# Performance work log

Hardware: AMD Instinct MI355X
Metric: run time of the kernel (lower is better)

## Reference

```python
import jax, jax.numpy as jnp
import numpy as np

K = 3  # kernel_size


def conv2d_same(x, w, b):
    # x: NHWC, w: HWIO
    y = jax.lax.conv_general_dilated(
        x, w, window_strides=(1, 1), padding='SAME',
        dimension_numbers=('NHWC', 'HWIO', 'NHWC'))
    return y + b


def setup_inputs() -> dict:
    key = jax.random.key(0)
    k0, k1, k2 = jax.random.split(key, 3)
    B, H, Wd, C, F = 8, 128, 128, 64, 128
    x = jax.random.normal(k0, (B, H, Wd, C), jnp.float32)
    # offset conv: small random weights (zeros in original init -> degenerate),
    # scaled down so offsets stay in a realistic few-pixel range
    W_off = jax.random.normal(k1, (K, K, C, 2 * K * K), jnp.float32) * 0.01
    b_off = jnp.zeros((2 * K * K,), jnp.float32)
    fan_in = K * K * K * K * C
    W = jax.random.normal(k2, (K, K, K * K * C, F), jnp.float32) / np.float32(np.sqrt(fan_in))
    b = jnp.zeros((F,), jnp.float32)
    return {"x": x, "W_off": W_off, "b_off": b_off, "W": W, "b": b}


def reference(x, W_off, b_off, W, b):
    B, H, Wd, C = x.shape
    KK = K * K
    # predicted per-pixel, per-tap (dx, dy) offsets
    offsets = conv2d_same(x, W_off, b_off).reshape(B, H, Wd, KK, 2)

    # base pixel grid, stacked as (x, y) like the original
    gy, gx = jnp.meshgrid(jnp.arange(H, dtype=jnp.float32),
                          jnp.arange(Wd, dtype=jnp.float32), indexing='ij')
    grid = jnp.stack([gx, gy], axis=-1)[None, :, :, None, :]  # (1,H,W,1,2)

    # kernel tap grid, 'xy' meshgrid like tf.meshgrid default
    off = (K - 1) / 2.0
    lin = jnp.linspace(-off, off, K).astype(jnp.float32)
    kx, ky = jnp.meshgrid(lin, lin)
    kgrid = jnp.stack([kx, ky], axis=-1).reshape(1, 1, 1, KK, 2)

    loc = grid + kgrid + offsets  # (B,H,W,KK,2)
    lx = jnp.clip(loc[..., 0], 0.0, Wd - 1.0)
    ly = jnp.clip(loc[..., 1], 0.0, H - 1.0)

    x0 = jnp.clip(jnp.floor(lx), 0.0, Wd - 1.0)
    x1 = jnp.clip(jnp.floor(lx) + 1.0, 0.0, Wd - 1.0)
    y0 = jnp.clip(jnp.floor(ly), 0.0, H - 1.0)
    y1 = jnp.clip(jnp.floor(ly) + 1.0, 0.0, H - 1.0)

    # weights computed from the CLIPPED corner coords, as in the original
    wa = (x1 - lx) * (y1 - ly)
    wb = (x1 - lx) * (ly - y0)
    wc = (lx - x0) * (y1 - ly)
    wd = (lx - x0) * (ly - y0)

    x0i, x1i = x0.astype(jnp.int32), x1.astype(jnp.int32)
    y0i, y1i = y0.astype(jnp.int32), y1.astype(jnp.int32)

    xf = x.reshape(B, H * Wd, C)

    def gather(yi, xi):
        idx = (yi * Wd + xi).reshape(B, -1)           # (B, H*W*KK)
        g = jax.vmap(lambda f, i: f[i])(xf, idx)      # (B, P, C)
        return g.reshape(B, H, Wd, KK, C)

    Ia = gather(y0i, x0i)
    Ib = gather(y1i, x0i)
    Ic = gather(y0i, x1i)
    Id = gather(y1i, x1i)

    sampled = (wa[..., None] * Ia + wb[..., None] * Ib
               + wc[..., None] * Ic + wd[..., None] * Id)
    sampled = sampled.reshape(B, H, Wd, KK * C)
    return conv2d_same(sampled, W, b)
```

## Files before the change

### kernel.cpp

```cpp
#include <hip/hip_runtime.h>
#include <hip/hip_bf16.h>

#define B_   8
#define H_   128
#define W_   128
#define C_   64
#define F_   128
#define KDIM 5184
#define BHW_ 131072

#define TH   8
#define TW   16
#define HY   10
#define HX   18
#define NPX  180

#define STILE 0
#define BTILE 11520
#define PARMW 36096
#define PARMO 37536
#define LDSSZ 38976

typedef __bf16 bf16x8 __attribute__((ext_vector_type(8)));
typedef float  f32x4  __attribute__((ext_vector_type(4)));

__device__ __forceinline__ unsigned short f2bf(float f) {
  unsigned int u = __float_as_uint(f);
  unsigned int r = (u + 0x7fffu + ((u >> 16) & 1u)) >> 16;
  return (unsigned short)r;
}

__global__ __launch_bounds__(256) void woff_prep_kernel(
    const float* __restrict__ Woff, unsigned short* __restrict__ WbHi,
    unsigned short* __restrict__ WbLo) {
  int u = blockIdx.x * 256 + threadIdx.x;
  if (u >= 18432) return;
  int j  = u & 7;
  int kq = (u >> 3) & 3;
  int n  = (u >> 5) & 15;
  int nt = (u >> 9) & 1;
  int tc = u >> 10;
  int tap = tc >> 1, kch = tc & 1;
  int o = nt * 16 + n;
  int c = kch * 32 + kq * 8 + j;
  float val = 0.f;
  if (o < 18) val = Woff[(tap * 64 + c) * 18 + o];
  unsigned short h = f2bf(val);
  float hf = __uint_as_float((unsigned)h << 16);
  WbHi[u] = h;
  WbLo[u] = f2bf(val - hf);
}

__global__ __launch_bounds__(256, 3) void offs_mfma_kernel(
    const float* __restrict__ x, const unsigned short* __restrict__ WbHi,
    const unsigned short* __restrict__ WbLo, const float* __restrict__ boff,
    float* __restrict__ offsP) {
  __shared__ __align__(16) short lds[26112];
  const int tid = threadIdx.x, lane = tid & 63, w = tid >> 6;
  const int bid = blockIdx.x;
  const int b  = bid >> 7;
  const int t  = bid & 127;
  const int r4 = t >> 2, cq = t & 3;
  const int gy0 = r4 * 4, gx0 = cq * 32;
  const float* xb = x + (size_t)b * (H_ * W_ * C_);

#pragma unroll
  for (int it = 0; it < 7; ++it) {
    int u = it * 256 + tid;
    if (u < 1632) {
      int p = u >> 3, j = u & 7;
      int rowi = p / 34, coli = p - rowi * 34;
      int gy = gy0 - 1 + rowi, gx = gx0 - 1 + coli;
      union { unsigned short s[8]; uint4 v; } hi, lo;
      if ((unsigned)gy < (unsigned)H_ && (unsigned)gx < (unsigned)W_) {
        const float* src = xb + (((gy << 7) + gx) << 6) + j * 8;
        float4 v0 = ((const float4*)src)[0], v1 = ((const float4*)src)[1];
        float f[8] = {v0.x, v0.y, v0.z, v0.w, v1.x, v1.y, v1.z, v1.w};
#pragma unroll
        for (int e = 0; e < 8; ++e) {
          unsigned short h16 = f2bf(f[e]);
          hi.s[e] = h16;
          lo.s[e] = f2bf(f[e] - __uint_as_float((unsigned)h16 << 16));
        }
      } else {
        hi.v = make_uint4(0, 0, 0, 0);
        lo.v = hi.v;
      }
      int a = p * 64 + ((j ^ (coli & 7)) * 8);
      *(uint4*)&lds[a] = hi.v;
      *(uint4*)&lds[13056 + a] = lo.v;
    }
  }
  __syncthreads();

  const int l15 = lane & 15, kq = lane >> 4;
  const int bbase = (l15 * 4 + kq) * 8;
  f32x4 acc[2][2] = {};

#pragma unroll
  for (int ky = 0; ky < 3; ++ky) {
#pragma unroll
    for (int kx = 0; kx < 3; ++kx) {
      const int tap = ky * 3 + kx;
#pragma unroll
      for (int kch = 0; kch < 2; ++kch) {
        const int tc = tap * 2 + kch;
        bf16x8 bh0 = *(const bf16x8*)&WbHi[tc * 1024 + bbase];
        bf16x8 bh1 = *(const bf16x8*)&WbHi[tc * 1024 + 512 + bbase];
        bf16x8 bl0 = *(const bf16x8*)&WbLo[tc * 1024 + bbase];
        bf16x8 bl1 = *(const bf16x8*)&WbLo[tc * 1024 + 512 + bbase];
#pragma unroll
        for (int mt = 0; mt < 2; ++mt) {
          int coli = mt * 16 + l15 + kx;
          int px = (w + ky) * 34 + coli;
          int a = px * 64 + (((kch * 4 + kq) ^ (coli & 7)) * 8);
          bf16x8 ah = *(const bf16x8*)&lds[a];
          bf16x8 al = *(const bf16x8*)&lds[13056 + a];
          acc[mt][0] = __builtin_amdgcn_mfma_f32_16x16x32_bf16(ah, bh0, acc[mt][0], 0, 0, 0);
          acc[mt][0] = __builtin_amdgcn_mfma_f32_16x16x32_bf16(al, bh0, acc[mt][0], 0, 0, 0);
          acc[mt][0] = __builtin_amdgcn_mfma_f32_16x16x32_bf16(ah, bl0, acc[mt][0], 0, 0, 0);
          acc[mt][1] = __builtin_amdgcn_mfma_f32_16x16x32_bf16(ah, bh1, acc[mt][1], 0, 0, 0);
          acc[mt][1] = __builtin_amdgcn_mfma_f32_16x16x32_bf16(al, bh1, acc[mt][1], 0, 0, 0);
          acc[mt][1] = __builtin_amdgcn_mfma_f32_16x16x32_bf16(ah, bl1, acc[mt][1], 0, 0, 0);
        }
      }
    }
  }

  __syncthreads();
  float* accbuf = (float*)lds;
  float bv0 = boff[l15];
  float bv1 = boff[min(16 + l15, 17)];
#pragma unroll
  for (int mt = 0; mt < 2; ++mt)
#pragma unroll
    for (int r = 0; r < 4; ++r) {
      int px = mt * 16 + kq * 4 + r;
      accbuf[(w * 32 + px) * 19 + l15] = acc[mt][0][r] + bv0;
      if (l15 < 2)
        accbuf[(w * 32 + px) * 19 + 16 + l15] = acc[mt][1][r] + bv1;
    }
  __syncthreads();
  const int lane32 = tid & 31, tpi = tid >> 5;
#pragma unroll
  for (int v = 0; v < 9; ++v) {
    int u = v * 8 + tpi;
    int o = u >> 2, w2 = u & 3;
    float val = accbuf[(w2 * 32 + lane32) * 19 + o];
    offsP[(size_t)o * BHW_ + (size_t)b * 16384 + (gy0 + w2) * 128 + gx0 + lane32] = val;
  }
}

__global__ __launch_bounds__(256) void wt_prep_kernel(
    const float* __restrict__ Wf, unsigned short* __restrict__ Wt) {
  __shared__ float Wl[64][65];
  const int tid = threadIdx.x;
  const int kk0 = (blockIdx.x % 81) * 64;
  const int f0  = (blockIdx.x / 81) * 64;
  for (int i = tid; i < 4096; i += 256) {
    int kk = i >> 6, f = i & 63;
    Wl[kk][f] = Wf[(size_t)(kk0 + kk) * F_ + f0 + f];
  }
  __syncthreads();
  for (int i = tid; i < 4096; i += 256) {
    int f = i >> 6, kk = i & 63;
    Wt[(size_t)(f0 + f) * KDIM + kk0 + kk] = f2bf(Wl[kk][f]);
  }
}

__global__ __launch_bounds__(256, 2) void fused_kernel(
    const float* __restrict__ x, const float* __restrict__ offsP,
    const unsigned short* __restrict__ Wt, const float* __restrict__ bias,
    float* __restrict__ out) {
  __shared__ __align__(16) short lds[LDSSZ];
  const int tid  = threadIdx.x;
  const int lane = tid & 63;
  const int wv   = tid >> 6;
  const int gr   = (blockIdx.x & 7) * 128 + (blockIdx.x >> 3);
  const int b    = gr >> 7;
  const int tile = gr & 127;
  const int ty   = tile >> 3, tx = tile & 7;
  const int gy0  = ty * TH, gx0 = tx * TW;
  const float* xb = x + (size_t)b * (H_ * W_ * C_);

  const int l15  = lane & 15, quad = lane >> 4;
  const int sub  = lane & 7,  rig  = lane >> 3;
  const int wn   = (wv & 1) * 64;

  f32x4 acc[4][4] = {};

  int p0[4];
#pragma unroll
  for (int i = 0; i < 4; ++i) p0[i] = ((wv >> 1) * 4 + i) * HX + l15;
  int bo[2][4];
#pragma unroll
  for (int ks = 0; ks < 2; ++ks)
#pragma unroll
    for (int j = 0; j < 4; ++j)
      bo[ks][j] = BTILE + (wn + 16 * j + l15) * 64 + (((ks * 4 + quad) ^ (l15 & 7)) * 8);

  const int s_py = tid / HX, s_px = tid - s_py * HX;

  for (int t = 0; t < 9; ++t) {
    __syncthreads();
#pragma unroll
    for (int i = 0; i < 12; ++i) {
      int slot = wv * 12 + i;
      int chunk = slot >> 4;
      int f = ((slot & 15) * 8) + rig;
      const short* src = (const short*)Wt + (size_t)f * KDIM +
                         chunk * 576 + t * 64 + ((sub ^ rig) * 8);
      __builtin_amdgcn_global_load_lds(
          (const __attribute__((address_space(1))) void*)src,
          (__attribute__((address_space(3))) void*)&lds[BTILE + slot * 512],
          16, 0, 0);
    }
    if (tid < NPX) {
      int gy = gy0 + s_py - 1, gx = gx0 + s_px - 1;
      float wa = 0.f, wb = 0.f, wc = 0.f, wd = 0.f;
      int oA = 0, oB = 0, oC = 0, oD = 0;
      if ((unsigned)gy < (unsigned)H_ && (unsigned)gx < (unsigned)W_) {
        int pix = (b * H_ + gy) * W_ + gx;
        float offx = offsP[(size_t)(2 * t) * BHW_ + pix];
        float offy = offsP[(size_t)(2 * t + 1) * BHW_ + pix];
        float lx = (float)gx + (float)(t % 3 - 1) + offx;
        float ly = (float)gy + (float)(t / 3 - 1) + offy;
        lx = fminf(fmaxf(lx, 0.f), 127.f);
        ly = fminf(fmaxf(ly, 0.f), 127.f);
        float fx = floorf(lx), fy = floorf(ly);
        float x0c = fminf(fmaxf(fx, 0.f), 127.f);
        float x1c = fminf(fmaxf(fx + 1.f, 0.f), 127.f);
        float y0c = fminf(fmaxf(fy, 0.f), 127.f);
        float y1c = fminf(fmaxf(fy + 1.f, 0.f), 127.f);
        wa = (x1c - lx) * (y1c - ly);
        wb = (x1c - lx) * (ly - y0c);
        wc = (lx - x0c) * (y1c - ly);
        wd = (lx - x0c) * (ly - y0c);
        int ix0 = (int)x0c, ix1 = (int)x1c, iy0 = (int)y0c, iy1 = (int)y1c;
        oA = (iy0 * W_ + ix0) * C_;
        oB = (iy1 * W_ + ix0) * C_;
        oC = (iy0 * W_ + ix1) * C_;
        oD = (iy1 * W_ + ix1) * C_;
      }
      ((float4*)&lds[PARMW])[tid] = make_float4(wa, wb, wc, wd);
      ((int4*)&lds[PARMO])[tid]  = make_int4(oA | (s_px << 20), oB, oC, oD);
    }
    __syncthreads();
#pragma unroll
    for (int it = 0; it < 6; ++it) {
      int u = it * 256 + tid;
      if (u < NPX * 8) {
        int p = u >> 3, j = u & 7;
        float4 wv4 = ((const float4*)&lds[PARMW])[p];
        int4   ov4 = ((const int4*)&lds[PARMO])[p];
        int pxl = ov4.x >> 20;
        const float* pa = xb + (ov4.x & 0xFFFFF) + j * 8;
        const float* pb = xb + ov4.y + j * 8;
        const float* pc = xb + ov4.z + j * 8;
        const float* pd = xb + ov4.w + j * 8;
        float4 A0 = ((const float4*)pa)[0], A1 = ((const float4*)pa)[1];
        float4 B0 = ((const float4*)pb)[0], B1 = ((const float4*)pb)[1];
        float4 C0 = ((const float4*)pc)[0], C1 = ((const float4*)pc)[1];
        float4 D0 = ((const float4*)pd)[0], D1 = ((const float4*)pd)[1];
        union { __bf16 h[8]; uint4 v; } uu;
        uu.h[0] = (__bf16)(wv4.x * A0.x + wv4.y * B0.x + wv4.z * C0.x + wv4.w * D0.x);
        uu.h[1] = (__bf16)(wv4.x * A0.y + wv4.y * B0.y + wv4.z * C0.y + wv4.w * D0.y);
        uu.h[2] = (__bf16)(wv4.x * A0.z + wv4.y * B0.z + wv4.z * C0.z + wv4.w * D0.z);
        uu.h[3] = (__bf16)(wv4.x * A0.w + wv4.y * B0.w + wv4.z * C0.w + wv4.w * D0.w);
        uu.h[4] = (__bf16)(wv4.x * A1.x + wv4.y * B1.x + wv4.z * C1.x + wv4.w * D1.x);
        uu.h[5] = (__bf16)(wv4.x * A1.y + wv4.y * B1.y + wv4.z * C1.y + wv4.w * D1.y);
        uu.h[6] = (__bf16)(wv4.x * A1.z + wv4.y * B1.z + wv4.z * C1.z + wv4.w * D1.z);
        uu.h[7] = (__bf16)(wv4.x * A1.w + wv4.y * B1.w + wv4.z * C1.w + wv4.w * D1.w);
        *(uint4*)&lds[STILE + p * 64 + ((j ^ (pxl & 7)) * 8)] = uu.v;
      }
    }
    __syncthreads();

    for (int g = 0; g < 3; ++g) {
      const int off2 = g * HX;
#pragma unroll
      for (int c3 = 0; c3 < 3; ++c3) {
        int t1 = (l15 + c3) & 7;
        int xr0 = ((quad ^ t1) * 8);
        int xr1 = (((4 + quad) ^ t1) * 8);
#pragma unroll
        for (int ks = 0; ks < 2; ++ks) {
          int xr = ks ? xr1 : xr0;
          bf16x8 af[4], bfr[4];
#pragma unroll
          for (int i = 0; i < 4; ++i)
            af[i] = *(const bf16x8*)&lds[(p0[i] + off2 + c3) * 64 + xr];
#pragma unroll
          for (int j = 0; j < 4; ++j)
            bfr[j] = *(const bf16x8*)&lds[bo[ks][j] + c3 * 8192];
#pragma unroll
          for (int i = 0; i < 4; ++i)
#pragma unroll
            for (int j = 0; j < 4; ++j)
              acc[i][j] = __builtin_amdgcn_mfma_f32_16x16x32_bf16(
                  af[i], bfr[j], acc[i][j], 0, 0, 0);
        }
      }
      if (g < 2) {
        __syncthreads();
#pragma unroll
        for (int i = 0; i < 12; ++i) {
          int slot = wv * 12 + i;
          int chunk = slot >> 4;
          int f = ((slot & 15) * 8) + rig;
          int tap2 = (g + 1) * 3 + chunk;
          const short* src = (const short*)Wt + (size_t)f * KDIM +
                             tap2 * 576 + t * 64 + ((sub ^ rig) * 8);
          __builtin_amdgcn_global_load_lds(
              (const __attribute__((address_space(1))) void*)src,
              (__attribute__((address_space(3))) void*)&lds[BTILE + slot * 512],
              16, 0, 0);
        }
        __syncthreads();
      }
    }
  }

  float bj[4];
#pragma unroll
  for (int j = 0; j < 4; ++j) bj[j] = bias[wn + 16 * j + l15];
#pragma unroll
  for (int i = 0; i < 4; ++i) {
    int gy = gy0 + (wv >> 1) * 4 + i;
#pragma unroll
    for (int r = 0; r < 4; ++r) {
      int gx = gx0 + quad * 4 + r;
      float* rp = out + ((size_t)((b * H_ + gy) * W_ + gx)) * F_;
#pragma unroll
      for (int j = 0; j < 4; ++j)
        rp[wn + 16 * j + l15] = acc[i][j][r] + bj[j];
    }
  }
}

extern "C" void kernel_launch(void* const* d_in, const int* in_sizes, int n_in,
                              void* d_out, int out_size, void* d_ws, size_t ws_size,
                              hipStream_t stream) {
  (void)in_sizes; (void)n_in; (void)out_size; (void)ws_size;
  const float* x    = (const float*)d_in[0];
  const float* Woff = (const float*)d_in[1];
  const float* boff = (const float*)d_in[2];
  const float* Wf   = (const float*)d_in[3];
  const float* bias = (const float*)d_in[4];
  float* out = (float*)d_out;

  char* ws = (char*)d_ws;
  size_t off_bytes = (size_t)18 * BHW_ * 4;
  size_t p1 = (off_bytes + 255) & ~(size_t)255;
  size_t wt_bytes = (size_t)F_ * KDIM * 2;
  float*          offsP = (float*)ws;
  unsigned short* Wt    = (unsigned short*)(ws + p1);
  unsigned short* WbHi  = (unsigned short*)(ws + p1 + wt_bytes);
  unsigned short* WbLo  = WbHi + 18432;

  woff_prep_kernel<<<72, 256, 0, stream>>>(Woff, WbHi, WbLo);
  offs_mfma_kernel<<<1024, 256, 0, stream>>>(x, WbHi, WbLo, boff, offsP);
  wt_prep_kernel<<<162, 256, 0, stream>>>(Wf, Wt);
  fused_kernel<<<1024, 256, 0, stream>>>(x, offsP, Wt, bias, out);
}
```

Before: 297.1 us.

## Merge prep kernels, use native bf16 casts, prefetch weight taps into registers

The two weight-preparation kernels are merged into a single launch that splits work by block index, removing one kernel launch. The offset kernel's hi/lo bf16 split now uses native __bf16 conversions instead of the manual rounding helper. In the fused kernel, the next weight-tap group is loaded from global memory into registers before the MFMA loop and written to LDS after the barrier, replacing the direct global-to-LDS loads so the global latency overlaps compute. The register prefetch uses 12 uint4 registers per thread, which can raise register pressure and hurt occupancy under the 2-wave launch bound.

Result: slower. 547.2 us (+84.2%).

```diff
diff --git a/kernel.cpp b/kernel.cpp
--- a/kernel.cpp
+++ b/kernel.cpp
@@ -30,25 +30,43 @@
   return (unsigned short)r;
 }
 
-__global__ __launch_bounds__(256) void woff_prep_kernel(
+__global__ __launch_bounds__(256) void prep_kernel(
     const float* __restrict__ Woff, unsigned short* __restrict__ WbHi,
-    unsigned short* __restrict__ WbLo) {
-  int u = blockIdx.x * 256 + threadIdx.x;
-  if (u >= 18432) return;
-  int j  = u & 7;
-  int kq = (u >> 3) & 3;
-  int n  = (u >> 5) & 15;
-  int nt = (u >> 9) & 1;
-  int tc = u >> 10;
-  int tap = tc >> 1, kch = tc & 1;
-  int o = nt * 16 + n;
-  int c = kch * 32 + kq * 8 + j;
-  float val = 0.f;
-  if (o < 18) val = Woff[(tap * 64 + c) * 18 + o];
-  unsigned short h = f2bf(val);
-  float hf = __uint_as_float((unsigned)h << 16);
-  WbHi[u] = h;
-  WbLo[u] = f2bf(val - hf);
+    unsigned short* __restrict__ WbLo, const float* __restrict__ Wf,
+    unsigned short* __restrict__ Wt) {
+  const int tid = threadIdx.x;
+  if (blockIdx.x < 72) {
+    int u = blockIdx.x * 256 + tid;
+    if (u >= 18432) return;
+    int j  = u & 7;
+    int kq = (u >> 3) & 3;
+    int n  = (u >> 5) & 15;
+    int nt = (u >> 9) & 1;
+    int tc = u >> 10;
+    int tap = tc >> 1, kch = tc & 1;
+    int o = nt * 16 + n;
+    int c = kch * 32 + kq * 8 + j;
+    float val = 0.f;
+    if (o < 18) val = Woff[(tap * 64 + c) * 18 + o];
+    unsigned short h = f2bf(val);
+    float hf = __uint_as_float((unsigned)h << 16);
+    WbHi[u] = h;
+    WbLo[u] = f2bf(val - hf);
+    return;
+  }
+  __shared__ float Wl[64][65];
+  const int bid = blockIdx.x - 72;
+  const int kk0 = (bid % 81) * 64;
+  const int f0  = (bid / 81) * 64;
+  for (int i = tid; i < 4096; i += 256) {
+    int kk = i >> 6, f = i & 63;
+    Wl[kk][f] = Wf[(size_t)(kk0 + kk) * F_ + f0 + f];
+  }
+  __syncthreads();
+  for (int i = tid; i < 4096; i += 256) {
+    int f = i >> 6, kk = i & 63;
+    Wt[(size_t)(f0 + f) * KDIM + kk0 + kk] = f2bf(Wl[kk][f]);
+  }
 }
 
 __global__ __launch_bounds__(256, 3) void offs_mfma_kernel(
@@ -71,16 +89,16 @@
       int p = u >> 3, j = u & 7;
       int rowi = p / 34, coli = p - rowi * 34;
       int gy = gy0 - 1 + rowi, gx = gx0 - 1 + coli;
-      union { unsigned short s[8]; uint4 v; } hi, lo;
+      union { __bf16 h[8]; uint4 v; } hi, lo;
       if ((unsigned)gy < (unsigned)H_ && (unsigned)gx < (unsigned)W_) {
         const float* src = xb + (((gy << 7) + gx) << 6) + j * 8;
         float4 v0 = ((const float4*)src)[0], v1 = ((const float4*)src)[1];
         float f[8] = {v0.x, v0.y, v0.z, v0.w, v1.x, v1.y, v1.z, v1.w};
 #pragma unroll
         for (int e = 0; e < 8; ++e) {
-          unsigned short h16 = f2bf(f[e]);
-          hi.s[e] = h16;
-          lo.s[e] = f2bf(f[e] - __uint_as_float((unsigned)h16 << 16));
+          __bf16 h16 = (__bf16)f[e];
+          hi.h[e] = h16;
+          lo.h[e] = (__bf16)(f[e] - (float)h16);
         }
       } else {
         hi.v = make_uint4(0, 0, 0, 0);
@@ -148,23 +166,6 @@
     int o = u >> 2, w2 = u & 3;
     float val = accbuf[(w2 * 32 + lane32) * 19 + o];
     offsP[(size_t)o * BHW_ + (size_t)b * 16384 + (gy0 + w2) * 128 + gx0 + lane32] = val;
-  }
-}
-
-__global__ __launch_bounds__(256) void wt_prep_kernel(
-    const float* __restrict__ Wf, unsigned short* __restrict__ Wt) {
-  __shared__ float Wl[64][65];
-  const int tid = threadIdx.x;
-  const int kk0 = (blockIdx.x % 81) * 64;
-  const int f0  = (blockIdx.x / 81) * 64;
-  for (int i = tid; i < 4096; i += 256) {
-    int kk = i >> 6, f = i & 63;
-    Wl[kk][f] = Wf[(size_t)(kk0 + kk) * F_ + f0 + f];
-  }
-  __syncthreads();
-  for (int i = tid; i < 4096; i += 256) {
-    int f = i >> 6, kk = i & 63;
-    Wt[(size_t)(f0 + f) * KDIM + kk0 + kk] = f2bf(Wl[kk][f]);
   }
 }
 
@@ -276,6 +277,15 @@
     }
     __syncthreads();
 
+    uint4 wreg[12];
+#pragma unroll
+    for (int i = 0; i < 12; ++i) {
+      int slot = wv * 12 + i;
+      int chunk = slot >> 4;
+      int f = ((slot & 15) * 8) + rig;
+      wreg[i] = *(const uint4*)((const short*)Wt + (size_t)f * KDIM +
+                                (3 + chunk) * 576 + t * 64 + ((sub ^ rig) * 8));
+    }
     for (int g = 0; g < 3; ++g) {
       const int off2 = g * HX;
 #pragma unroll
@@ -306,15 +316,18 @@
 #pragma unroll
         for (int i = 0; i < 12; ++i) {
           int slot = wv * 12 + i;
-          int chunk = slot >> 4;
-          int f = ((slot & 15) * 8) + rig;
-          int tap2 = (g + 1) * 3 + chunk;
-          const short* src = (const short*)Wt + (size_t)f * KDIM +
-                             tap2 * 576 + t * 64 + ((sub ^ rig) * 8);
-          __builtin_amdgcn_global_load_lds(
-              (const __attribute__((address_space(1))) void*)src,
-              (__attribute__((address_space(3))) void*)&lds[BTILE + slot * 512],
-              16, 0, 0);
+          *(uint4*)&lds[BTILE + slot * 512 + lane * 8] = wreg[i];
+        }
+        if (g == 0) {
+#pragma unroll
+          for (int i = 0; i < 12; ++i) {
+            int slot = wv * 12 + i;
+            int chunk = slot >> 4;
+            int f = ((slot & 15) * 8) + rig;
+            wreg[i] = *(const uint4*)((const short*)Wt + (size_t)f * KDIM +
+                                      (6 + chunk) * 576 + t * 64 +
+                                      ((sub ^ rig) * 8));
+          }
         }
         __syncthreads();
       }
@@ -358,8 +371,7 @@
   unsigned short* WbHi  = (unsigned short*)(ws + p1 + wt_bytes);
   unsigned short* WbLo  = WbHi + 18432;
 
-  woff_prep_kernel<<<72, 256, 0, stream>>>(Woff, WbHi, WbLo);
+  prep_kernel<<<234, 256, 0, stream>>>(Woff, WbHi, WbLo, Wf, Wt);
   offs_mfma_kernel<<<1024, 256, 0, stream>>>(x, WbHi, WbLo, boff, offsP);
-  wt_prep_kernel<<<162, 256, 0, stream>>>(Wf, Wt);
   fused_kernel<<<1024, 256, 0, stream>>>(x, offsP, Wt, bias, out);
 }
```
